# Performance work log

Measured on AMD Instinct MI355X. Metric: run time of the kernel, lower is better.

Reference implementation:

```python
import jax, jax.numpy as jnp
import numpy as np

N, H, DDE, NH = 256, 256, 64, 4

def setup_inputs() -> dict:
    key = jax.random.key(0)
    ks = jax.random.split(key, 12)
    rn = lambda k, s, sc=1.0: (jax.random.normal(k, s) * sc).astype(jnp.float32)
    return {
        "action_hidden_state": rn(ks[0], (N, H)),
        "goal_hidden_state": rn(ks[1], (N, H)),
        "goal": rn(ks[2], (N, 2)),
        "action": rn(ks[3], (N, 2)),
        "W_dist": rn(ks[4], (8, DDE), 0.3),          # distEmbedding Linear(8, dde)
        "b_dist": jnp.zeros((DDE,), jnp.float32),
        "W_gate": rn(ks[5], (DDE, H), 0.1),          # gateFC Linear(dde, H)
        "b_gate": jnp.zeros((H,), jnp.float32),
        "w": rn(ks[6], (NH, 1, H, H), 0.06),         # GAT per-head projection
        "a": rn(ks[7], (1, 1, 2 * H, 1), 0.06),      # attention vector
        "bias": jnp.zeros((H,), jnp.float32),
    }

def reference(action_hidden_state, goal_hidden_state, goal, action,
              W_dist, b_dist, W_gate, b_gate, w, a, bias):
    n = goal.shape[0]
    # --- InteractionGate.cal_gate: x1[i,j] = x[j], x2[i,j] = x[i] ---
    g1 = jnp.broadcast_to(goal[None, :, :], (n, n, 2))
    g2 = jnp.broadcast_to(goal[:, None, :], (n, n, 2))
    a1 = jnp.broadcast_to(action[None, :, :], (n, n, 2))
    a2 = jnp.broadcast_to(action[:, None, :], (n, n, 2))
    dist = jnp.concatenate([a2, g2, a1, g1], axis=-1)                 # [n,n,8]
    gate = jax.nn.sigmoid(jax.nn.relu(dist @ W_dist + b_dist) @ W_gate + b_gate)  # [n,n,H]
    # temp_action_1[i,j] = action_hidden_state[j]
    gate_action = gate * jnp.tanh(action_hidden_state[None, :, :])    # [n,n,H]
    # diagonal entries replaced by goal_hidden_state (mask_goal = eye)
    eye = jnp.eye(n, dtype=bool)[:, :, None]
    gated_h = jnp.where(eye, goal_hidden_state[None, :, :], gate_action)  # [n,n,H]

    # --- GAT assembly: h_self[i,k] = ahs[i]; h_other = cat(ahs, gated_h) ---
    h_other = jnp.concatenate([action_hidden_state[:, None, :], gated_h], axis=1)  # [n,n+1,H]

    wm = w[:, 0]          # [NH,H,H]
    a_flat = a[0, 0, :, 0]  # [2H]
    f = wm.shape[-1]
    n_head = wm.shape[0]
    # h_self rows along k are all identical -> project once per (head, node)
    hsp = jnp.einsum('nh,zhf->znf', action_hidden_state, wm)          # [NH,n,f]
    hop = jnp.einsum('nkh,zhf->znkf', h_other, wm)                    # [NH,n,n+1,f]
    # cat([h_self', h_other']) @ a  ==  h_self'@a[:f] + h_other'@a[f:]
    score = (hsp @ a_flat[:f])[:, :, None] + hop @ a_flat[f:]         # [NH,n,n+1]
    e = jnp.where(score > 0, score, 0.2 * score)                      # LeakyReLU(0.2)
    alpha = jax.nn.softmax(e, axis=-1)                                # softmax over neighbors
    # h_attn = matmul(h_other, w) == hop; weighted sum over k, mean over heads
    out = jnp.einsum('znk,znkf->nf', alpha, hop) / n_head             # [n,f]
    return jax.nn.relu(out) + bias
```

## Files before the change

kernel.cpp:

```cpp
#include <hip/hip_runtime.h>
#include <hip/hip_bf16.h>

#define NN 256
#define HH 256

typedef __attribute__((ext_vector_type(8))) short short8;
typedef __attribute__((ext_vector_type(4))) float f32x4;

__device__ __forceinline__ ushort f2bf(float x) {
    __hip_bfloat16 h = __float2bfloat16(x);
    return *reinterpret_cast<ushort*>(&h);
}
template <int CTRL>
__device__ __forceinline__ float dpp_add(float x) {
    int y = __builtin_amdgcn_update_dpp(0, __float_as_int(x), CTRL, 0xF, 0xF, true);
    return x + __int_as_float(y);
}
__device__ __forceinline__ float red16(float v) {
    v = dpp_add<0xB1>(v);
    v = dpp_add<0x4E>(v);
    v = dpp_add<0x141>(v);
    v = dpp_add<0x140>(v);
    return v;
}

#define WS_P   0
#define WS_Q   16384
#define WS_T   32768
#define WS_WA  98304
#define WS_WB  99328
#define WS_WGT 100352
#define WS_PV  104448
#define WS_ML  628736

__global__ __launch_bounds__(256) void precompute_kernel(
    const float* __restrict__ ahs, const float* __restrict__ goal,
    const float* __restrict__ action, const float* __restrict__ Wd,
    const float* __restrict__ b_dist, const float* __restrict__ Wg,
    const float* __restrict__ w, const float* __restrict__ a,
    float* __restrict__ ws)
{
    const int b = blockIdx.x;
    const int t = threadIdx.x;
    float* P  = ws + WS_P;
    float* Q  = ws + WS_Q;
    float* T  = ws + WS_T;
    float* WA = ws + WS_WA;
    float* WB = ws + WS_WB;
    ushort* WgT = (ushort*)(ws + WS_WGT);

    if (b < NN) {
        T[b*HH + t] = tanhf(ahs[b*HH + t]);
        if (t < 64) {
            float a0 = action[2*b], a1 = action[2*b+1];
            float g0 = goal[2*b],   g1 = goal[2*b+1];
            P[b*64 + t] = a0*Wd[0*64+t] + a1*Wd[1*64+t]
                        + g0*Wd[2*64+t] + g1*Wd[3*64+t] + b_dist[t];
            Q[b*64 + t] = a0*Wd[4*64+t] + a1*Wd[5*64+t]
                        + g0*Wd[6*64+t] + g1*Wd[7*64+t];
        }
    } else if (b < NN + 16) {
        const int r    = b - NN;
        const int z    = r >> 2;
        const int rg   = r & 3;
        const int wid  = t >> 6;
        const int lane = t & 63;
        const int hbase = rg*64 + wid*16;
        const f32x4 aB = *(const f32x4*)(a + lane*4);
        const f32x4 aA = *(const f32x4*)(a + HH + lane*4);
#pragma unroll 4
        for (int rr = 0; rr < 16; ++rr) {
            const int h = hbase + rr;
            const f32x4 w4 = *(const f32x4*)(w + z*HH*HH + h*HH + lane*4);
            float dA = w4.x*aA.x + w4.y*aA.y + w4.z*aA.z + w4.w*aA.w;
            float dB = w4.x*aB.x + w4.y*aB.y + w4.z*aB.z + w4.w*aB.w;
#pragma unroll
            for (int off = 32; off; off >>= 1) {
                dA += __shfl_xor(dA, off);
                dB += __shfl_xor(dB, off);
            }
            if (lane == 0) { WA[z*HH + h] = dA; WB[z*HH + h] = dB; }
        }
    } else {
#pragma unroll 8
        for (int d = 0; d < 64; ++d) WgT[t*64 + d] = f2bf(Wg[d*HH + t]);
    }
}

__global__ __launch_bounds__(256) void gat_partial_kernel(
    const float* __restrict__ ahs, const float* __restrict__ ghs,
    const float* __restrict__ b_gate, float* __restrict__ ws)
{
    const int n    = blockIdx.x & 255;
    const int half = blockIdx.x >> 8;
    const int t    = threadIdx.x;
    const int wid  = t >> 6;
    const int lane = t & 63;
    const int quad = lane >> 4;
    const int l15  = lane & 15;
    const int n0   = wid * 64;

    const float* P  = ws + WS_P;
    const float* Q  = ws + WS_Q;
    const float* T  = ws + WS_T;
    const float* WA = ws + WS_WA;
    const float* WB = ws + WS_WB;
    const ushort* WgT = (const ushort*)(ws + WS_WGT);
    float* PV = ws + WS_PV;
    float* ML = ws + WS_ML;

    __shared__ ushort hidb[32][72];
    __shared__ __align__(16) float part[4][32][4];
    __shared__ __align__(16) float alpha_s[32][4];
    __shared__ __align__(16) float scl4[4];
    __shared__ float m_s[4], l_s[4], cz_s[4];
    __shared__ float vred[4][4][260];

    int hcol[4];
#pragma unroll
    for (int nt = 0; nt < 4; ++nt) hcol[nt] = n0 + nt*16 + l15;

    short8 bfrag[4][2];
    float  wa_reg[4][4];
    float  bgv[4];
#pragma unroll
    for (int nt = 0; nt < 4; ++nt) {
#pragma unroll
        for (int kh = 0; kh < 2; ++kh)
            bfrag[nt][kh] = *(const short8*)(WgT + hcol[nt]*64 + kh*32 + quad*8);
#pragma unroll
        for (int z = 0; z < 4; ++z) wa_reg[z][nt] = WA[z*HH + hcol[nt]];
        bgv[nt] = b_gate[hcol[nt]];
    }

    float vacc[4][4];
    {
        float av[4];
#pragma unroll
        for (int nt = 0; nt < 4; ++nt) av[nt] = ahs[n*HH + hcol[nt]];
#pragma unroll
        for (int z = 0; z < 4; ++z)
#pragma unroll
            for (int nt = 0; nt < 4; ++nt)
                vacc[z][nt] = (half == 0 && quad == 0) ? av[nt] : 0.f;
    }

    const int jj_own = t >> 3;
    const int db     = (t & 7) * 8;
    float pn[8];
#pragma unroll
    for (int i = 0; i < 8; ++i) pn[i] = P[n*64 + db + i];

    {
        float pc = 0.f, ps = 0.f;
        for (int h = lane; h < HH; h += 64) {
            float av = ahs[n*HH + h];
            pc = fmaf(av, WB[wid*HH + h], pc);
            ps = fmaf(av, WA[wid*HH + h], ps);
        }
#pragma unroll
        for (int off = 32; off; off >>= 1) {
            pc += __shfl_xor(pc, off);
            ps += __shfl_xor(ps, off);
        }
        if (lane == 0) {
            cz_s[wid] = pc;
            if (half == 0) {
                float sc = pc + ps;
                float e0 = sc > 0.f ? sc : 0.2f * sc;
                m_s[wid] = e0;
                l_s[wid] = 1.0f;
            } else {
                m_s[wid] = -__builtin_inff();
                l_s[wid] = 0.0f;
            }
        }
    }
    __syncthreads();

    for (int cc = 0; cc < 4; ++cc) {
        const int j0 = half*128 + cc*32;

        float tval[2][4][4];
#pragma unroll
        for (int mt = 0; mt < 2; ++mt)
#pragma unroll
            for (int r = 0; r < 4; ++r) {
                const int jg = j0 + mt*16 + quad*4 + r;
#pragma unroll
                for (int nt = 0; nt < 4; ++nt)
                    tval[mt][nt][r] = T[jg*HH + hcol[nt]];
            }

        {
            const int j = j0 + jj_own;
            const float4 qa = *(const float4*)(Q + j*64 + db);
            const float4 qb = *(const float4*)(Q + j*64 + db + 4);
            ushort hv[8];
            hv[0] = f2bf(fmaxf(pn[0] + qa.x, 0.f));
            hv[1] = f2bf(fmaxf(pn[1] + qa.y, 0.f));
            hv[2] = f2bf(fmaxf(pn[2] + qa.z, 0.f));
            hv[3] = f2bf(fmaxf(pn[3] + qa.w, 0.f));
            hv[4] = f2bf(fmaxf(pn[4] + qb.x, 0.f));
            hv[5] = f2bf(fmaxf(pn[5] + qb.y, 0.f));
            hv[6] = f2bf(fmaxf(pn[6] + qb.z, 0.f));
            hv[7] = f2bf(fmaxf(pn[7] + qb.w, 0.f));
            *(short8*)&hidb[jj_own][db] = *(short8*)hv;
        }
        __syncthreads();

        f32x4 acc[2][4];
#pragma unroll
        for (int mt = 0; mt < 2; ++mt)
#pragma unroll
            for (int nt = 0; nt < 4; ++nt) acc[mt][nt] = (f32x4){0.f,0.f,0.f,0.f};

        short8 afrag[2][2];
#pragma unroll
        for (int mt = 0; mt < 2; ++mt)
#pragma unroll
            for (int kh = 0; kh < 2; ++kh)
                afrag[mt][kh] = *(const short8*)&hidb[mt*16 + l15][kh*32 + quad*8];

#pragma unroll
        for (int mt = 0; mt < 2; ++mt)
#pragma unroll
            for (int nt = 0; nt < 4; ++nt) {
                acc[mt][nt] = __builtin_amdgcn_mfma_f32_16x16x32_bf16(
                    afrag[mt][0], bfrag[nt][0], acc[mt][nt], 0, 0, 0);
                acc[mt][nt] = __builtin_amdgcn_mfma_f32_16x16x32_bf16(
                    afrag[mt][1], bfrag[nt][1], acc[mt][nt], 0, 0, 0);
            }

        float vals[2][4][4];
        float pp[4][2][4];
#pragma unroll
        for (int z = 0; z < 4; ++z)
#pragma unroll
            for (int mt = 0; mt < 2; ++mt)
#pragma unroll
                for (int r = 0; r < 4; ++r) pp[z][mt][r] = 0.f;

#pragma unroll
        for (int mt = 0; mt < 2; ++mt) {
#pragma unroll
            for (int r = 0; r < 4; ++r) {
                const int jg = j0 + mt*16 + quad*4 + r;
                const bool diag = (jg == n);
#pragma unroll
                for (int nt = 0; nt < 4; ++nt) {
                    float u = acc[mt][nt][r] + bgv[nt];
                    float val;
                    if (diag) {
                        val = ghs[n*HH + hcol[nt]];
                    } else {
                        float g = 1.0f / (1.0f + __expf(-u));
                        val = g * tval[mt][nt][r];
                    }
                    vals[mt][nt][r] = val;
                    pp[0][mt][r] = fmaf(val, wa_reg[0][nt], pp[0][mt][r]);
                    pp[1][mt][r] = fmaf(val, wa_reg[1][nt], pp[1][mt][r]);
                    pp[2][mt][r] = fmaf(val, wa_reg[2][nt], pp[2][mt][r]);
                    pp[3][mt][r] = fmaf(val, wa_reg[3][nt], pp[3][mt][r]);
                }
            }
        }
#pragma unroll
        for (int z = 0; z < 4; ++z)
#pragma unroll
            for (int mt = 0; mt < 2; ++mt)
#pragma unroll
                for (int r = 0; r < 4; ++r)
                    pp[z][mt][r] = red16(pp[z][mt][r]);
        if (l15 == 0) {
#pragma unroll
            for (int z = 0; z < 4; ++z)
#pragma unroll
                for (int mt = 0; mt < 2; ++mt)
#pragma unroll
                    for (int r = 0; r < 4; ++r)
                        part[z][mt*16 + quad*4 + r][wid] = pp[z][mt][r];
        }
        __syncthreads();

        {
            const int jj = lane & 31;
            f32x4 pr = *(const f32x4*)&part[wid][jj][0];
            const bool act = lane < 32;
            float s = cz_s[wid] + ((pr.x + pr.y) + (pr.z + pr.w));
            float e = act ? (s > 0.f ? s : 0.2f * s) : -__builtin_inff();
            float mx = e;
#pragma unroll
            for (int off = 32; off; off >>= 1) mx = fmaxf(mx, __shfl_xor(mx, off));
            float m_old = m_s[wid];
            float m_new = fmaxf(m_old, mx);
            float at = act ? __expf(e - m_new) : 0.f;
            float ss = at;
#pragma unroll
            for (int off = 32; off; off >>= 1) ss += __shfl_xor(ss, off);
            if (act) alpha_s[jj][wid] = at;
            if (lane == 0) {
                float scale = __expf(m_old - m_new);
                scl4[wid] = scale;
                l_s[wid]  = l_s[wid] * scale + ss;
                m_s[wid]  = m_new;
            }
        }
        __syncthreads();

        {
            f32x4 scv = *(const f32x4*)&scl4[0];
            float s0 = scv.x, s1 = scv.y, s2 = scv.z, s3 = scv.w;
#pragma unroll
            for (int nt = 0; nt < 4; ++nt) {
                vacc[0][nt] *= s0; vacc[1][nt] *= s1;
                vacc[2][nt] *= s2; vacc[3][nt] *= s3;
            }
#pragma unroll
            for (int mt = 0; mt < 2; ++mt)
#pragma unroll
                for (int r = 0; r < 4; ++r) {
                    f32x4 al = *(const f32x4*)&alpha_s[mt*16 + quad*4 + r][0];
#pragma unroll
                    for (int nt = 0; nt < 4; ++nt) {
                        float v = vals[mt][nt][r];
                        vacc[0][nt] = fmaf(al.x, v, vacc[0][nt]);
                        vacc[1][nt] = fmaf(al.y, v, vacc[1][nt]);
                        vacc[2][nt] = fmaf(al.z, v, vacc[2][nt]);
                        vacc[3][nt] = fmaf(al.w, v, vacc[3][nt]);
                    }
                }
        }
    }

#pragma unroll
    for (int z = 0; z < 4; ++z)
#pragma unroll
        for (int nt = 0; nt < 4; ++nt)
            vred[quad][z][hcol[nt]] = vacc[z][nt];
    __syncthreads();
#pragma unroll
    for (int z = 0; z < 4; ++z) {
        float s = (vred[0][z][t] + vred[1][z][t]) + (vred[2][z][t] + vred[3][z][t]);
        PV[((half*4 + z)*NN + n)*HH + t] = s;
    }
    if (lane == 0) {
        ML[((half*4 + wid)*NN + n)*2 + 0] = m_s[wid];
        ML[((half*4 + wid)*NN + n)*2 + 1] = l_s[wid];
    }
}

__global__ __launch_bounds__(256) void gat_combine_kernel(
    const float* __restrict__ w, const float* __restrict__ bias,
    const float* __restrict__ ws, float* __restrict__ out)
{
    const int n = blockIdx.x;
    const int t = threadIdx.x;
    const float* PV = ws + WS_PV;
    const float* ML = ws + WS_ML;

    __shared__ float vfin[4][256];

#pragma unroll
    for (int z = 0; z < 4; ++z) {
        float mA = ML[((0*4 + z)*NN + n)*2 + 0];
        float lA = ML[((0*4 + z)*NN + n)*2 + 1];
        float mB = ML[((1*4 + z)*NN + n)*2 + 0];
        float lB = ML[((1*4 + z)*NN + n)*2 + 1];
        float m  = fmaxf(mA, mB);
        float sA = __expf(mA - m);
        float sB = __expf(mB - m);
        float inv = 1.0f / (lA*sA + lB*sB);
        float vA = PV[((0*4 + z)*NN + n)*HH + t];
        float vB = PV[((1*4 + z)*NN + n)*HH + t];
        vfin[z][t] = (vA*sA + vB*sB) * inv;
    }
    __syncthreads();

    float res = 0.f;
#pragma unroll
    for (int z = 0; z < 4; ++z) {
        const float* wz = w + z*HH*HH + t;
        float a0 = 0.f, a1 = 0.f;
        for (int h = 0; h < HH; h += 8) {
            float l0 = wz[(h+0)*HH], l1 = wz[(h+1)*HH];
            float l2 = wz[(h+2)*HH], l3 = wz[(h+3)*HH];
            float l4 = wz[(h+4)*HH], l5 = wz[(h+5)*HH];
            float l6 = wz[(h+6)*HH], l7 = wz[(h+7)*HH];
            f32x4 v0 = *(const f32x4*)&vfin[z][h];
            f32x4 v1 = *(const f32x4*)&vfin[z][h+4];
            a0 = fmaf(l0, v0.x, a0); a1 = fmaf(l1, v0.y, a1);
            a0 = fmaf(l2, v0.z, a0); a1 = fmaf(l3, v0.w, a1);
            a0 = fmaf(l4, v1.x, a0); a1 = fmaf(l5, v1.y, a1);
            a0 = fmaf(l6, v1.z, a0); a1 = fmaf(l7, v1.w, a1);
        }
        res += a0 + a1;
    }
    res = fmaxf(res * 0.25f, 0.f) + bias[t];
    out[n*HH + t] = res;
}

extern "C" void kernel_launch(void* const* d_in, const int* in_sizes, int n_in,
                              void* d_out, int out_size, void* d_ws, size_t ws_size,
                              hipStream_t stream)
{
    const float* ahs    = (const float*)d_in[0];
    const float* ghs    = (const float*)d_in[1];
    const float* goal   = (const float*)d_in[2];
    const float* action = (const float*)d_in[3];
    const float* Wd     = (const float*)d_in[4];
    const float* b_dist = (const float*)d_in[5];
    const float* Wg     = (const float*)d_in[6];
    const float* b_gate = (const float*)d_in[7];
    const float* w      = (const float*)d_in[8];
    const float* a      = (const float*)d_in[9];
    const float* bias   = (const float*)d_in[10];
    float* ws   = (float*)d_ws;
    float* outp = (float*)d_out;

    precompute_kernel<<<273, 256, 0, stream>>>(ahs, goal, action, Wd, b_dist, Wg, w, a, ws);
    gat_partial_kernel<<<512, 256, 0, stream>>>(ahs, ghs, b_gate, ws);
    gat_combine_kernel<<<256, 256, 0, stream>>>(w, bias, ws, outp);
}
```

Baseline: 126.2 us.

## Split attention over four key-chunks and parallelize final projection across blocks

The partial kernel now splits the 256 neighbors into four chunks of 64 per node instead of two halves, launching 1024 blocks with 16-row MFMA tiles, smaller shared buffers and a launch bound targeting higher occupancy. T values are loaded inside the epilogue instead of being prefetched into registers. A new merge kernel combines the four softmax partials into a normalized per-head vector. The combine kernel is restructured so each block handles two nodes and a 64-column slice, with K split across waves. The aim is more parallelism and less register pressure, at the cost of an extra launch and extra workspace traffic.

```diff
diff --git a/kernel.cpp b/kernel.cpp
--- a/kernel.cpp
+++ b/kernel.cpp
@@ -5,6 +5,7 @@
 #define HH 256
 
 typedef __attribute__((ext_vector_type(8))) short short8;
+typedef __attribute__((ext_vector_type(4))) short s16x4;
 typedef __attribute__((ext_vector_type(4))) float f32x4;
 
 __device__ __forceinline__ ushort f2bf(float x) {
@@ -31,7 +32,8 @@
 #define WS_WB  99328
 #define WS_WGT 100352
 #define WS_PV  104448
-#define WS_ML  628736
+#define WS_ML  1153024
+#define WS_VN  1161216
 
 __global__ __launch_bounds__(256) void precompute_kernel(
     const float* __restrict__ ahs, const float* __restrict__ goal,
@@ -87,12 +89,12 @@
     }
 }
 
-__global__ __launch_bounds__(256) void gat_partial_kernel(
+__global__ __launch_bounds__(256, 4) void gat_partial_kernel(
     const float* __restrict__ ahs, const float* __restrict__ ghs,
     const float* __restrict__ b_gate, float* __restrict__ ws)
 {
     const int n    = blockIdx.x & 255;
-    const int half = blockIdx.x >> 8;
+    const int qq   = blockIdx.x >> 8;
     const int t    = threadIdx.x;
     const int wid  = t >> 6;
     const int lane = t & 63;
@@ -109,9 +111,9 @@
     float* PV = ws + WS_PV;
     float* ML = ws + WS_ML;
 
-    __shared__ ushort hidb[32][72];
-    __shared__ __align__(16) float part[4][32][4];
-    __shared__ __align__(16) float alpha_s[32][4];
+    __shared__ ushort hidb[16][72];
+    __shared__ __align__(16) float part[4][16][4];
+    __shared__ __align__(16) float alpha_s[16][4];
     __shared__ __align__(16) float scl4[4];
     __shared__ float m_s[4], l_s[4], cz_s[4];
     __shared__ float vred[4][4][260];
@@ -142,14 +144,14 @@
         for (int z = 0; z < 4; ++z)
 #pragma unroll
             for (int nt = 0; nt < 4; ++nt)
-                vacc[z][nt] = (half == 0 && quad == 0) ? av[nt] : 0.f;
-    }
-
-    const int jj_own = t >> 3;
-    const int db     = (t & 7) * 8;
-    float pn[8];
-#pragma unroll
-    for (int i = 0; i < 8; ++i) pn[i] = P[n*64 + db + i];
+                vacc[z][nt] = (qq == 0 && quad == 0) ? av[nt] : 0.f;
+    }
+
+    const int jj_own = t >> 4;
+    const int db     = (t & 15) * 4;
+    float pn[4];
+#pragma unroll
+    for (int i = 0; i < 4; ++i) pn[i] = P[n*64 + db + i];
 
     {
         float pc = 0.f, ps = 0.f;
@@ -165,7 +167,7 @@
         }
         if (lane == 0) {
             cz_s[wid] = pc;
-            if (half == 0) {
+            if (qq == 0) {
                 float sc = pc + ps;
                 float e0 = sc > 0.f ? sc : 0.2f * sc;
                 m_s[wid] = e0;
@@ -179,125 +181,87 @@
     __syncthreads();
 
     for (int cc = 0; cc < 4; ++cc) {
-        const int j0 = half*128 + cc*32;
-
-        float tval[2][4][4];
-#pragma unroll
-        for (int mt = 0; mt < 2; ++mt)
-#pragma unroll
-            for (int r = 0; r < 4; ++r) {
-                const int jg = j0 + mt*16 + quad*4 + r;
-#pragma unroll
-                for (int nt = 0; nt < 4; ++nt)
-                    tval[mt][nt][r] = T[jg*HH + hcol[nt]];
-            }
+        const int j0 = qq*64 + cc*16;
 
         {
             const int j = j0 + jj_own;
             const float4 qa = *(const float4*)(Q + j*64 + db);
-            const float4 qb = *(const float4*)(Q + j*64 + db + 4);
-            ushort hv[8];
+            ushort hv[4];
             hv[0] = f2bf(fmaxf(pn[0] + qa.x, 0.f));
             hv[1] = f2bf(fmaxf(pn[1] + qa.y, 0.f));
             hv[2] = f2bf(fmaxf(pn[2] + qa.z, 0.f));
             hv[3] = f2bf(fmaxf(pn[3] + qa.w, 0.f));
-            hv[4] = f2bf(fmaxf(pn[4] + qb.x, 0.f));
-            hv[5] = f2bf(fmaxf(pn[5] + qb.y, 0.f));
-            hv[6] = f2bf(fmaxf(pn[6] + qb.z, 0.f));
-            hv[7] = f2bf(fmaxf(pn[7] + qb.w, 0.f));
-            *(short8*)&hidb[jj_own][db] = *(short8*)hv;
+            *(s16x4*)&hidb[jj_own][db] = *(s16x4*)hv;
         }
         __syncthreads();
 
-        f32x4 acc[2][4];
-#pragma unroll
-        for (int mt = 0; mt < 2; ++mt)
-#pragma unroll
-            for (int nt = 0; nt < 4; ++nt) acc[mt][nt] = (f32x4){0.f,0.f,0.f,0.f};
-
-        short8 afrag[2][2];
-#pragma unroll
-        for (int mt = 0; mt < 2; ++mt)
-#pragma unroll
-            for (int kh = 0; kh < 2; ++kh)
-                afrag[mt][kh] = *(const short8*)&hidb[mt*16 + l15][kh*32 + quad*8];
-
-#pragma unroll
-        for (int mt = 0; mt < 2; ++mt)
+        f32x4 acc[4];
+#pragma unroll
+        for (int nt = 0; nt < 4; ++nt) acc[nt] = (f32x4){0.f,0.f,0.f,0.f};
+        short8 afrag[2];
+#pragma unroll
+        for (int kh = 0; kh < 2; ++kh)
+            afrag[kh] = *(const short8*)&hidb[l15][kh*32 + quad*8];
+#pragma unroll
+        for (int nt = 0; nt < 4; ++nt) {
+            acc[nt] = __builtin_amdgcn_mfma_f32_16x16x32_bf16(
+                afrag[0], bfrag[nt][0], acc[nt], 0, 0, 0);
+            acc[nt] = __builtin_amdgcn_mfma_f32_16x16x32_bf16(
+                afrag[1], bfrag[nt][1], acc[nt], 0, 0, 0);
+        }
+
+        float vals[4][4];
+#pragma unroll
+        for (int r = 0; r < 4; ++r) {
+            const int jg = j0 + quad*4 + r;
+            const bool diag = (jg == n);
 #pragma unroll
             for (int nt = 0; nt < 4; ++nt) {
-                acc[mt][nt] = __builtin_amdgcn_mfma_f32_16x16x32_bf16(
-                    afrag[mt][0], bfrag[nt][0], acc[mt][nt], 0, 0, 0);
-                acc[mt][nt] = __builtin_amdgcn_mfma_f32_16x16x32_bf16(
-                    afrag[mt][1], bfrag[nt][1], acc[mt][nt], 0, 0, 0);
-            }
-
-        float vals[2][4][4];
-        float pp[4][2][4];
-#pragma unroll
-        for (int z = 0; z < 4; ++z)
-#pragma unroll
-            for (int mt = 0; mt < 2; ++mt)
-#pragma unroll
-                for (int r = 0; r < 4; ++r) pp[z][mt][r] = 0.f;
-
-#pragma unroll
-        for (int mt = 0; mt < 2; ++mt) {
+                float u = acc[nt][r] + bgv[nt];
+                float val;
+                if (diag) {
+                    val = ghs[n*HH + hcol[nt]];
+                } else {
+                    float g = 1.0f / (1.0f + __expf(-u));
+                    val = g * T[jg*HH + hcol[nt]];
+                }
+                vals[nt][r] = val;
+            }
+        }
+#pragma unroll
+        for (int z = 0; z < 4; ++z) {
+            float pp[4];
 #pragma unroll
             for (int r = 0; r < 4; ++r) {
-                const int jg = j0 + mt*16 + quad*4 + r;
-                const bool diag = (jg == n);
-#pragma unroll
-                for (int nt = 0; nt < 4; ++nt) {
-                    float u = acc[mt][nt][r] + bgv[nt];
-                    float val;
-                    if (diag) {
-                        val = ghs[n*HH + hcol[nt]];
-                    } else {
-                        float g = 1.0f / (1.0f + __expf(-u));
-                        val = g * tval[mt][nt][r];
-                    }
-                    vals[mt][nt][r] = val;
-                    pp[0][mt][r] = fmaf(val, wa_reg[0][nt], pp[0][mt][r]);
-                    pp[1][mt][r] = fmaf(val, wa_reg[1][nt], pp[1][mt][r]);
-                    pp[2][mt][r] = fmaf(val, wa_reg[2][nt], pp[2][mt][r]);
-                    pp[3][mt][r] = fmaf(val, wa_reg[3][nt], pp[3][mt][r]);
-                }
-            }
-        }
-#pragma unroll
-        for (int z = 0; z < 4; ++z)
-#pragma unroll
-            for (int mt = 0; mt < 2; ++mt)
+                float s = 0.f;
+#pragma unroll
+                for (int nt = 0; nt < 4; ++nt)
+                    s = fmaf(vals[nt][r], wa_reg[z][nt], s);
+                pp[r] = red16(s);
+            }
+            if (l15 == 0) {
 #pragma unroll
                 for (int r = 0; r < 4; ++r)
-                    pp[z][mt][r] = red16(pp[z][mt][r]);
-        if (l15 == 0) {
-#pragma unroll
-            for (int z = 0; z < 4; ++z)
-#pragma unroll
-                for (int mt = 0; mt < 2; ++mt)
-#pragma unroll
-                    for (int r = 0; r < 4; ++r)
-                        part[z][mt*16 + quad*4 + r][wid] = pp[z][mt][r];
+                    part[z][quad*4 + r][wid] = pp[r];
+            }
         }
         __syncthreads();
 
         {
-            const int jj = lane & 31;
+            const int jj = lane & 15;
             f32x4 pr = *(const f32x4*)&part[wid][jj][0];
-            const bool act = lane < 32;
+            const bool act = lane < 16;
             float s = cz_s[wid] + ((pr.x + pr.y) + (pr.z + pr.w));
             float e = act ? (s > 0.f ? s : 0.2f * s) : -__builtin_inff();
             float mx = e;
 #pragma unroll
-            for (int off = 32; off; off >>= 1) mx = fmaxf(mx, __shfl_xor(mx, off));
+            for (int off = 8; off; off >>= 1) mx = fmaxf(mx, __shfl_xor(mx, off));
             float m_old = m_s[wid];
             float m_new = fmaxf(m_old, mx);
             float at = act ? __expf(e - m_new) : 0.f;
             float ss = at;
 #pragma unroll
-            for (int off = 32; off; off >>= 1) ss += __shfl_xor(ss, off);
+            for (int off = 8; off; off >>= 1) ss += __shfl_xor(ss, off);
             if (act) alpha_s[jj][wid] = at;
             if (lane == 0) {
                 float scale = __expf(m_old - m_new);
@@ -310,26 +274,23 @@
 
         {
             f32x4 scv = *(const f32x4*)&scl4[0];
-            float s0 = scv.x, s1 = scv.y, s2 = scv.z, s3 = scv.w;
 #pragma unroll
             for (int nt = 0; nt < 4; ++nt) {
-                vacc[0][nt] *= s0; vacc[1][nt] *= s1;
-                vacc[2][nt] *= s2; vacc[3][nt] *= s3;
-            }
-#pragma unroll
-            for (int mt = 0; mt < 2; ++mt)
-#pragma unroll
-                for (int r = 0; r < 4; ++r) {
-                    f32x4 al = *(const f32x4*)&alpha_s[mt*16 + quad*4 + r][0];
-#pragma unroll
-                    for (int nt = 0; nt < 4; ++nt) {
-                        float v = vals[mt][nt][r];
-                        vacc[0][nt] = fmaf(al.x, v, vacc[0][nt]);
-                        vacc[1][nt] = fmaf(al.y, v, vacc[1][nt]);
-                        vacc[2][nt] = fmaf(al.z, v, vacc[2][nt]);
-                        vacc[3][nt] = fmaf(al.w, v, vacc[3][nt]);
-                    }
+                vacc[0][nt] *= scv.x; vacc[1][nt] *= scv.y;
+                vacc[2][nt] *= scv.z; vacc[3][nt] *= scv.w;
+            }
+#pragma unroll
+            for (int r = 0; r < 4; ++r) {
+                f32x4 al = *(const f32x4*)&alpha_s[quad*4 + r][0];
+#pragma unroll
+                for (int nt = 0; nt < 4; ++nt) {
+                    float v = vals[nt][r];
+                    vacc[0][nt] = fmaf(al.x, v, vacc[0][nt]);
+                    vacc[1][nt] = fmaf(al.y, v, vacc[1][nt]);
+                    vacc[2][nt] = fmaf(al.z, v, vacc[2][nt]);
+                    vacc[3][nt] = fmaf(al.w, v, vacc[3][nt]);
                 }
+            }
         }
     }
 
@@ -342,62 +303,81 @@
 #pragma unroll
     for (int z = 0; z < 4; ++z) {
         float s = (vred[0][z][t] + vred[1][z][t]) + (vred[2][z][t] + vred[3][z][t]);
-        PV[((half*4 + z)*NN + n)*HH + t] = s;
+        PV[((qq*4 + z)*NN + n)*HH + t] = s;
     }
     if (lane == 0) {
-        ML[((half*4 + wid)*NN + n)*2 + 0] = m_s[wid];
-        ML[((half*4 + wid)*NN + n)*2 + 1] = l_s[wid];
-    }
-}
-
-__global__ __launch_bounds__(256) void gat_combine_kernel(
-    const float* __restrict__ w, const float* __restrict__ bias,
-    const float* __restrict__ ws, float* __restrict__ out)
+        ML[((qq*4 + wid)*NN + n)*2 + 0] = m_s[wid];
+        ML[((qq*4 + wid)*NN + n)*2 + 1] = l_s[wid];
+    }
+}
+
+__global__ __launch_bounds__(256) void gat_merge_kernel(float* __restrict__ ws)
 {
     const int n = blockIdx.x;
     const int t = threadIdx.x;
     const float* PV = ws + WS_PV;
     const float* ML = ws + WS_ML;
-
-    __shared__ float vfin[4][256];
-
+    float* VN = ws + WS_VN;
+
+    __shared__ float sq[4][4];
+    if (t < 4) {
+        float m[4], l[4];
+#pragma unroll
+        for (int q = 0; q < 4; ++q) {
+            m[q] = ML[((q*4 + t)*NN + n)*2 + 0];
+            l[q] = ML[((q*4 + t)*NN + n)*2 + 1];
+        }
+        float mm = fmaxf(fmaxf(m[0], m[1]), fmaxf(m[2], m[3]));
+        float s0 = __expf(m[0]-mm), s1 = __expf(m[1]-mm);
+        float s2 = __expf(m[2]-mm), s3 = __expf(m[3]-mm);
+        float inv = 1.0f / (l[0]*s0 + l[1]*s1 + l[2]*s2 + l[3]*s3);
+        sq[t][0] = s0*inv; sq[t][1] = s1*inv; sq[t][2] = s2*inv; sq[t][3] = s3*inv;
+    }
+    __syncthreads();
 #pragma unroll
     for (int z = 0; z < 4; ++z) {
-        float mA = ML[((0*4 + z)*NN + n)*2 + 0];
-        float lA = ML[((0*4 + z)*NN + n)*2 + 1];
-        float mB = ML[((1*4 + z)*NN + n)*2 + 0];
-        float lB = ML[((1*4 + z)*NN + n)*2 + 1];
-        float m  = fmaxf(mA, mB);
-        float sA = __expf(mA - m);
-        float sB = __expf(mB - m);
-        float inv = 1.0f / (lA*sA + lB*sB);
-        float vA = PV[((0*4 + z)*NN + n)*HH + t];
-        float vB = PV[((1*4 + z)*NN + n)*HH + t];
-        vfin[z][t] = (vA*sA + vB*sB) * inv;
-    }
+        float v = 0.f;
+#pragma unroll
+        for (int q = 0; q < 4; ++q)
+            v = fmaf(sq[z][q], PV[((q*4 + z)*NN + n)*HH + t], v);
+        VN[n*1024 + z*HH + t] = v;
+    }
+}
+
+__global__ __launch_bounds__(256) void gat_combine_kernel(
+    const float* __restrict__ w, const float* __restrict__ bias,
+    const float* __restrict__ ws, float* __restrict__ out)
+{
+    const int n0  = (blockIdx.x >> 2) * 2;
+    const int f0  = (blockIdx.x & 3) * 64;
+    const int t   = threadIdx.x;
+    const int wid = t >> 6;
+    const int lane= t & 63;
+    const int ni  = wid & 1;
+    const int ko  = wid >> 1;
+    const float* VN = ws + WS_VN;
+
+    __shared__ float accL[2][64];
+
+    const int row = __builtin_amdgcn_readfirstlane(n0 + ni);
+    const float* vrow = VN + row*1024 + ko*512;
+    const float* wp   = w + (ko*512)*HH + f0 + lane;
+
+    float a0=0.f, a1=0.f, a2=0.f, a3=0.f;
+#pragma unroll 8
+    for (int k = 0; k < 512; k += 4) {
+        a0 = fmaf(vrow[k+0], wp[(size_t)(k+0)*HH], a0);
+        a1 = fmaf(vrow[k+1], wp[(size_t)(k+1)*HH], a1);
+        a2 = fmaf(vrow[k+2], wp[(size_t)(k+2)*HH], a2);
+        a3 = fmaf(vrow[k+3], wp[(size_t)(k+3)*HH], a3);
+    }
+    float acc = (a0+a1)+(a2+a3);
+    if (ko == 1) accL[ni][lane] = acc;
     __syncthreads();
-
-    float res = 0.f;
-#pragma unroll
-    for (int z = 0; z < 4; ++z) {
-        const float* wz = w + z*HH*HH + t;
-        float a0 = 0.f, a1 = 0.f;
-        for (int h = 0; h < HH; h += 8) {
-            float l0 = wz[(h+0)*HH], l1 = wz[(h+1)*HH];
-            float l2 = wz[(h+2)*HH], l3 = wz[(h+3)*HH];
-            float l4 = wz[(h+4)*HH], l5 = wz[(h+5)*HH];
-            float l6 = wz[(h+6)*HH], l7 = wz[(h+7)*HH];
-            f32x4 v0 = *(const f32x4*)&vfin[z][h];
-            f32x4 v1 = *(const f32x4*)&vfin[z][h+4];
-            a0 = fmaf(l0, v0.x, a0); a1 = fmaf(l1, v0.y, a1);
-            a0 = fmaf(l2, v0.z, a0); a1 = fmaf(l3, v0.w, a1);
-            a0 = fmaf(l4, v1.x, a0); a1 = fmaf(l5, v1.y, a1);
-            a0 = fmaf(l6, v1.z, a0); a1 = fmaf(l7, v1.w, a1);
-        }
-        res += a0 + a1;
-    }
-    res = fmaxf(res * 0.25f, 0.f) + bias[t];
-    out[n*HH + t] = res;
+    if (ko == 0) {
+        float tot = acc + accL[ni][lane];
+        out[(n0+ni)*HH + f0 + lane] = fmaxf(0.25f*tot, 0.f) + bias[f0+lane];
+    }
 }
 
 extern "C" void kernel_launch(void* const* d_in, const int* in_sizes, int n_in,
@@ -419,6 +399,7 @@
     float* outp = (float*)d_out;
 
     precompute_kernel<<<273, 256, 0, stream>>>(ahs, goal, action, Wd, b_dist, Wg, w, a, ws);
-    gat_partial_kernel<<<512, 256, 0, stream>>>(ahs, ghs, b_gate, ws);
-    gat_combine_kernel<<<256, 256, 0, stream>>>(w, bias, ws, outp);
-}
+    gat_partial_kernel<<<1024, 256, 0, stream>>>(ahs, ghs, b_gate, ws);
+    gat_merge_kernel<<<256, 256, 0, stream>>>(ws);
+    gat_combine_kernel<<<512, 256, 0, stream>>>(w, bias, ws, outp);
+}
```

Result: slower. 142.6 us (+13.0%).
